# Optimization experiments

Measured on AMD Instinct MI355X. Metric: run time of the kernel, lower is better.

The kernel has to match this reference:

```python
import math
import jax, jax.numpy as jnp
import numpy as np

B, T, C, H = 2, 2048, 1024, 16  # batch, seq, embed, heads; head_dim = C//H = 64

def setup_inputs() -> dict:
    key = jax.random.key(0)
    k1, k2, k3 = jax.random.split(key, 3)
    x = jax.random.normal(k1, (B, T, C), dtype=jnp.float32)
    w_qkv = jax.random.normal(k2, (C, 3 * C), dtype=jnp.float32) * 0.02
    b_qkv = jnp.zeros((3 * C,), dtype=jnp.float32)
    w_proj = jax.random.normal(k3, (C, C), dtype=jnp.float32) * (0.02 / math.sqrt(2 * 24))
    b_proj = jnp.zeros((C,), dtype=jnp.float32)
    return {"x": x, "w_qkv": w_qkv, "b_qkv": b_qkv, "w_proj": w_proj, "b_proj": b_proj}

def reference(x, w_qkv, b_qkv, w_proj, b_proj):
    b, t, c = x.shape
    h = H
    qkv = x @ w_qkv + b_qkv  # [b, t, 3c]
    q, k, v = jnp.split(qkv, 3, axis=-1)
    # [b, t, c] -> [b, h, t, d]
    def heads(z):
        return z.reshape(b, t, h, c // h).transpose(0, 2, 1, 3)
    q, k, v = heads(q), heads(k), heads(v)
    # NOTE: source scales by sqrt(c) (full embed dim), not sqrt(head_dim)
    att = jnp.einsum("bhqd,bhkd->bhqk", q, k) / math.sqrt(c)
    # causal mask: -inf above diagonal
    mask = jnp.triu(jnp.full((t, t), -jnp.inf, dtype=att.dtype), k=1)
    att = att + mask
    att = jax.nn.softmax(att, axis=-1)
    out = jnp.einsum("bhqk,bhkd->bhqd", att, v)  # [b, h, t, d]
    out = out.transpose(0, 2, 1, 3).reshape(b, t, c)
    return out @ w_proj + b_proj
```

## Files before the change

kernel.cpp:

```cpp
#include <hip/hip_runtime.h>
#include <math.h>

#define BSZ 2
#define TSEQ 2048
#define CEMB 1024
#define NHEAD 16
#define HDIM 64

typedef float f32x4 __attribute__((ext_vector_type(4)));
typedef short bf16x8 __attribute__((ext_vector_type(8)));

typedef __attribute__((address_space(3))) char lds_char;
typedef __attribute__((address_space(1))) const char gbl_char;

__device__ __forceinline__ void g2l16(const void* g, void* l) {
    __builtin_amdgcn_global_load_lds((const gbl_char*)g, (lds_char*)l, 16, 0, 0);
}

__device__ __forceinline__ unsigned short f2bf(float x) {
    unsigned u = __float_as_uint(x);
    unsigned r = ((u >> 16) & 1u) + 0x7fffu;
    return (unsigned short)((u + r) >> 16);
}

__global__ __launch_bounds__(256) void conv_f32_bf16(
    const float* __restrict__ in, unsigned short* __restrict__ out)
{
    size_t i = ((size_t)blockIdx.x * 256 + threadIdx.x) * 8;
    float4 a = *(const float4*)(in + i);
    float4 b = *(const float4*)(in + i + 4);
    union { unsigned short u[8]; uint4 v; } pk;
    pk.u[0] = f2bf(a.x); pk.u[1] = f2bf(a.y); pk.u[2] = f2bf(a.z); pk.u[3] = f2bf(a.w);
    pk.u[4] = f2bf(b.x); pk.u[5] = f2bf(b.y); pk.u[6] = f2bf(b.z); pk.u[7] = f2bf(b.w);
    *(uint4*)(out + i) = pk.v;
}

__global__ __launch_bounds__(256) void conv_transpose_bf16(
    const float* __restrict__ w, unsigned short* __restrict__ wT, int K, int N)
{
    __shared__ float t[32][33];
    const int n0 = blockIdx.x * 32, k0 = blockIdx.y * 32;
    const int tx = threadIdx.x & 31, ty = threadIdx.x >> 5;
    #pragma unroll
    for (int i = 0; i < 4; ++i)
        t[ty + i * 8][tx] = w[(size_t)(k0 + ty + i * 8) * N + n0 + tx];
    __syncthreads();
    #pragma unroll
    for (int i = 0; i < 4; ++i) {
        int r = ty + i * 8;
        wT[(size_t)(n0 + r) * K + k0 + tx] = f2bf(t[tx][r]);
    }
}

template <int EPI>
__global__ __launch_bounds__(256) void gemm_mfma(
    const unsigned short* __restrict__ A, const unsigned short* __restrict__ BT,
    const float* __restrict__ bias,
    unsigned short* __restrict__ qo, unsigned short* __restrict__ ko,
    unsigned short* __restrict__ vo, float* __restrict__ fo,
    int M, int N, int K)
{
    __shared__ __align__(16) char sA[128 * 64 * 2];
    __shared__ __align__(16) char sB[128 * 64 * 2];

    const int tid = threadIdx.x;
    const int lane = tid & 63;
    const int wid = tid >> 6;
    const int wm = wid >> 1, wn = wid & 1;
    const int row0 = blockIdx.y * 128;
    const int col0 = blockIdx.x * 128;

    f32x4 acc[4][4] = {};

    for (int k0 = 0; k0 < K; k0 += 64) {
        __syncthreads();
        #pragma unroll
        for (int i = 0; i < 4; ++i) {
            int cid = i * 256 + tid;
            int row = cid >> 3, c2 = cid & 7;
            g2l16(&A[(size_t)(row0 + row) * K + k0 + ((c2 ^ (row & 7)) << 3)],
                  sA + ((i * 256 + (tid & 192)) << 4));
        }
        #pragma unroll
        for (int i = 0; i < 4; ++i) {
            int cid = i * 256 + tid;
            int row = cid >> 3, c2 = cid & 7;
            g2l16(&BT[(size_t)(col0 + row) * K + k0 + ((c2 ^ (row & 7)) << 3)],
                  sB + ((i * 256 + (tid & 192)) << 4));
        }
        __syncthreads();

        #pragma unroll
        for (int ks = 0; ks < 2; ++ks) {
            bf16x8 af[4], bf[4];
            #pragma unroll
            for (int mi = 0; mi < 4; ++mi) {
                int row = wm * 64 + mi * 16 + (lane & 15);
                int ch = ((lane >> 4) + 4 * ks) ^ (row & 7);
                af[mi] = *(const bf16x8*)(sA + row * 128 + (ch << 4));
            }
            #pragma unroll
            for (int ni = 0; ni < 4; ++ni) {
                int row = wn * 64 + ni * 16 + (lane & 15);
                int ch = ((lane >> 4) + 4 * ks) ^ (row & 7);
                bf[ni] = *(const bf16x8*)(sB + row * 128 + (ch << 4));
            }
            #pragma unroll
            for (int mi = 0; mi < 4; ++mi)
                #pragma unroll
                for (int ni = 0; ni < 4; ++ni)
                    acc[mi][ni] = __builtin_amdgcn_mfma_f32_16x16x32_bf16(
                        af[mi], bf[ni], acc[mi][ni], 0, 0, 0);
        }
    }

    #pragma unroll
    for (int mi = 0; mi < 4; ++mi) {
        const int rg = row0 + wm * 64 + mi * 16 + (lane >> 4) * 4;
        #pragma unroll
        for (int ni = 0; ni < 4; ++ni) {
            const int cg = col0 + wn * 64 + ni * 16 + (lane & 15);
            const float bv = bias[cg];
            if (EPI == 1) {
                #pragma unroll
                for (int r = 0; r < 4; ++r)
                    fo[(size_t)(rg + r) * N + cg] = acc[mi][ni][r] + bv;
            } else {
                const int region = col0 >> 10;
                if (region < 2) {
                    unsigned short* dst = region ? ko : qo;
                    const int nn = cg - (region << 10);
                    #pragma unroll
                    for (int r = 0; r < 4; ++r)
                        dst[(size_t)(rg + r) * CEMB + nn] = f2bf(acc[mi][ni][r] + bv);
                } else {
                    const int nloc = cg - 2048;
                    const int h = nloc >> 6, d = nloc & 63;
                    const int b = rg >> 11, t = rg & 2047;
                    ushort4 pk;
                    pk.x = f2bf(acc[mi][ni][0] + bv);
                    pk.y = f2bf(acc[mi][ni][1] + bv);
                    pk.z = f2bf(acc[mi][ni][2] + bv);
                    pk.w = f2bf(acc[mi][ni][3] + bv);
                    *(ushort4*)&vo[(((size_t)b * NHEAD + h) * HDIM + d) * TSEQ + t] = pk;
                }
            }
        }
    }
}

__global__ __launch_bounds__(256) void flash_mfma(
    const unsigned short* __restrict__ qb, const unsigned short* __restrict__ kb,
    const unsigned short* __restrict__ vt, unsigned short* __restrict__ ob)
{
    const int u = blockIdx.x >> 5;
    const int bh = blockIdx.x & 31;
    const int qt = (u & 1) ? (31 - (u >> 1)) : (u >> 1);
    const int b = bh >> 4, h = bh & 15;
    const int q0 = qt * 64;

    __shared__ __align__(16) char sQ[8192];
    __shared__ __align__(16) char sK[8192];
    __shared__ __align__(16) char sV[8192];
    __shared__ __align__(16) char sP[8192];

    const int tid = threadIdx.x;
    const int lane = tid & 63;
    const int wid = tid >> 6;
    const int g = lane >> 4;
    const int lr = lane & 15;
    const int q7 = lr & 7;

    #pragma unroll
    for (int i = 0; i < 2; ++i) {
        int cid = i * 256 + tid;
        int row = cid >> 3, c2 = cid & 7;
        g2l16(&qb[(size_t)(b * TSEQ + q0 + row) * CEMB + h * HDIM + ((c2 ^ (row & 7)) << 3)],
              sQ + ((i * 256 + (tid & 192)) << 4));
    }

    f32x4 o[4] = {};
    float mrow = -INFINITY, lrow = 0.f;
    const float c = 0.0450744431f;

    for (int kt = 0; kt <= qt; ++kt) {
        const int k0 = kt * 64;
        __syncthreads();
        #pragma unroll
        for (int i = 0; i < 2; ++i) {
            int cid = i * 256 + tid;
            int row = cid >> 3, c2 = cid & 7;
            g2l16(&kb[(size_t)(b * TSEQ + k0 + row) * CEMB + h * HDIM + ((c2 ^ (row & 7)) << 3)],
                  sK + ((i * 256 + (tid & 192)) << 4));
        }
        #pragma unroll
        for (int i = 0; i < 2; ++i) {
            int cid = i * 256 + tid;
            int row = cid >> 3, c2 = cid & 7;
            g2l16(&vt[(((size_t)b * NHEAD + h) * HDIM + row) * TSEQ + k0 + ((c2 ^ (row & 7)) << 3)],
                  sV + ((i * 256 + (tid & 192)) << 4));
        }
        __syncthreads();

        bf16x8 qf[2];
        #pragma unroll
        for (int ks = 0; ks < 2; ++ks) {
            int row = wid * 16 + lr;
            int ch = (g + 4 * ks) ^ q7;
            qf[ks] = *(const bf16x8*)(sQ + row * 128 + (ch << 4));
        }
        f32x4 s[4] = {};
        #pragma unroll
        for (int ni = 0; ni < 4; ++ni) {
            #pragma unroll
            for (int ks = 0; ks < 2; ++ks) {
                int row = ni * 16 + lr;
                int ch = (g + 4 * ks) ^ q7;
                bf16x8 kf = *(const bf16x8*)(sK + row * 128 + (ch << 4));
                s[ni] = __builtin_amdgcn_mfma_f32_16x16x32_bf16(kf, qf[ks], s[ni], 0, 0, 0);
            }
        }

        #pragma unroll
        for (int ni = 0; ni < 4; ++ni)
            #pragma unroll
            for (int r = 0; r < 4; ++r)
                s[ni][r] *= c;
        const int qrow_g = q0 + wid * 16 + lr;
        if (kt == qt) {
            #pragma unroll
            for (int ni = 0; ni < 4; ++ni)
                #pragma unroll
                for (int r = 0; r < 4; ++r)
                    if (k0 + ni * 16 + g * 4 + r > qrow_g) s[ni][r] = -INFINITY;
        }

        f32x4 m01, m23;
        #pragma unroll
        for (int r = 0; r < 4; ++r) {
            m01[r] = fmaxf(s[0][r], s[1][r]);
            m23[r] = fmaxf(s[2][r], s[3][r]);
        }
        float v = fmaxf(fmaxf(fmaxf(m01[0], m23[0]), fmaxf(m01[1], m23[1])),
                        fmaxf(fmaxf(m01[2], m23[2]), fmaxf(m01[3], m23[3])));
        v = fmaxf(v, __shfl_xor(v, 16));
        v = fmaxf(v, __shfl_xor(v, 32));

        if (!__all(v <= mrow + 8.f)) {
            const float mnew = fmaxf(mrow, v);
            const float sc = exp2f(mrow - mnew);
            lrow *= sc;
            #pragma unroll
            for (int ni = 0; ni < 4; ++ni)
                #pragma unroll
                for (int r = 0; r < 4; ++r)
                    o[ni][r] *= sc;
            mrow = mnew;
        }

        float ps = 0.f;
        #pragma unroll
        for (int ni = 0; ni < 4; ++ni) {
            ushort4 pk;
            #pragma unroll
            for (int r = 0; r < 4; ++r) {
                const float p = exp2f(s[ni][r] - mrow);
                ps += p;
                ((unsigned short*)&pk)[r] = f2bf(p);
            }
            const int ch = (2 * ni + (g >> 1)) ^ q7;
            *(uint2*)(sP + (wid * 16 + lr) * 128 + (ch << 4) + ((g & 1) << 3)) =
                *(const uint2*)&pk;
        }
        ps += __shfl_xor(ps, 16);
        ps += __shfl_xor(ps, 32);
        lrow += ps;

        asm volatile("s_waitcnt lgkmcnt(0)" ::: "memory");

        bf16x8 pf[2];
        #pragma unroll
        for (int ks = 0; ks < 2; ++ks) {
            int ch = (g + 4 * ks) ^ q7;
            pf[ks] = *(const bf16x8*)(sP + (wid * 16 + lr) * 128 + (ch << 4));
        }
        #pragma unroll
        for (int ni = 0; ni < 4; ++ni) {
            #pragma unroll
            for (int ks = 0; ks < 2; ++ks) {
                int row = ni * 16 + lr;
                int ch = (g + 4 * ks) ^ q7;
                bf16x8 vf = *(const bf16x8*)(sV + row * 128 + (ch << 4));
                o[ni] = __builtin_amdgcn_mfma_f32_16x16x32_bf16(vf, pf[ks], o[ni], 0, 0, 0);
            }
        }
    }

    const float linv = 1.f / lrow;
    __syncthreads();
    #pragma unroll
    for (int ni = 0; ni < 4; ++ni) {
        ushort4 pk;
        #pragma unroll
        for (int r = 0; r < 4; ++r)
            ((unsigned short*)&pk)[r] = f2bf(o[ni][r] * linv);
        const int ch = (2 * ni + (g >> 1)) ^ q7;
        *(uint2*)(sP + (wid * 16 + lr) * 128 + (ch << 4) + ((g & 1) << 3)) =
            *(const uint2*)&pk;
    }
    __syncthreads();
    #pragma unroll
    for (int i = 0; i < 2; ++i) {
        const int cid = i * 256 + tid;
        const int row = cid >> 3;
        const int ch = cid & 7;
        uint4 val = *(const uint4*)(sP + row * 128 + ((ch ^ (row & 7)) << 4));
        *(uint4*)&ob[(size_t)(b * TSEQ + q0 + row) * CEMB + h * HDIM + ch * 8] = val;
    }
}

extern "C" void kernel_launch(void* const* d_in, const int* in_sizes, int n_in,
                              void* d_out, int out_size, void* d_ws, size_t ws_size,
                              hipStream_t stream)
{
    (void)in_sizes; (void)n_in; (void)out_size; (void)ws_size;

    const float* x      = (const float*)d_in[0];
    const float* w_qkv  = (const float*)d_in[1];
    const float* b_qkv  = (const float*)d_in[2];
    const float* w_proj = (const float*)d_in[3];
    const float* b_proj = (const float*)d_in[4];
    float* out = (float*)d_out;

    const int M = BSZ * TSEQ;
    unsigned short* xb     = (unsigned short*)d_ws;
    unsigned short* wqkvT  = xb     + (size_t)M * CEMB;
    unsigned short* wprojT = wqkvT  + (size_t)3 * CEMB * CEMB;
    unsigned short* qbuf   = wprojT + (size_t)CEMB * CEMB;
    unsigned short* kbuf   = qbuf   + (size_t)M * CEMB;
    unsigned short* vbuf   = kbuf   + (size_t)M * CEMB;
    unsigned short* attb   = vbuf   + (size_t)M * CEMB;

    conv_f32_bf16<<<dim3((M * CEMB) / 2048), 256, 0, stream>>>(x, xb);
    conv_transpose_bf16<<<dim3(3 * CEMB / 32, CEMB / 32), 256, 0, stream>>>(
        w_qkv, wqkvT, CEMB, 3 * CEMB);
    conv_transpose_bf16<<<dim3(CEMB / 32, CEMB / 32), 256, 0, stream>>>(
        w_proj, wprojT, CEMB, CEMB);

    gemm_mfma<0><<<dim3(3 * CEMB / 128, M / 128), 256, 0, stream>>>(
        xb, wqkvT, b_qkv, qbuf, kbuf, vbuf, nullptr, M, 3 * CEMB, CEMB);

    flash_mfma<<<dim3(32 * 32), 256, 0, stream>>>(qbuf, kbuf, vbuf, attb);

    gemm_mfma<1><<<dim3(CEMB / 128, M / 128), 256, 0, stream>>>(
        attb, wprojT, b_proj, nullptr, nullptr, nullptr, out, M, CEMB, CEMB);
}
```

Measured before the change: 196.3 us.

## Double-buffer K/V tiles in flash attention and fold softmax scale into Q

The flash attention kernel now double-buffers the K and V tiles in LDS, prefetching the next tile while computing on the current one, with one barrier per iteration. Q fragments are loaded once into registers, reusing the sP buffer for staging. The softmax scale is folded into Q in the QKV GEMM epilogue, and the bf16 packing uses the hardware v_cvt_pk_bf16_f32 instruction. The block-index mapping is also reordered to change how causal query tiles spread across CUs. LDS use rises and the overlap depends on correct waits for the asynchronous global-to-LDS loads.

```diff
diff --git a/kernel.cpp b/kernel.cpp
--- a/kernel.cpp
+++ b/kernel.cpp
@@ -21,6 +21,12 @@
     unsigned u = __float_as_uint(x);
     unsigned r = ((u >> 16) & 1u) + 0x7fffu;
     return (unsigned short)((u + r) >> 16);
+}
+
+__device__ __forceinline__ unsigned pkbf(float lo, float hi) {
+    unsigned r;
+    asm("v_cvt_pk_bf16_f32 %0, %1, %2" : "=v"(r) : "v"(lo), "v"(hi));
+    return r;
 }
 
 __global__ __launch_bounds__(256) void conv_f32_bf16(
@@ -129,10 +135,11 @@
                 const int region = col0 >> 10;
                 if (region < 2) {
                     unsigned short* dst = region ? ko : qo;
+                    const float sc = region ? 1.f : 0.0450744431f;
                     const int nn = cg - (region << 10);
                     #pragma unroll
                     for (int r = 0; r < 4; ++r)
-                        dst[(size_t)(rg + r) * CEMB + nn] = f2bf(acc[mi][ni][r] + bv);
+                        dst[(size_t)(rg + r) * CEMB + nn] = f2bf((acc[mi][ni][r] + bv) * sc);
                 } else {
                     const int nloc = cg - 2048;
                     const int h = nloc >> 6, d = nloc & 63;
@@ -153,15 +160,18 @@
     const unsigned short* __restrict__ qb, const unsigned short* __restrict__ kb,
     const unsigned short* __restrict__ vt, unsigned short* __restrict__ ob)
 {
-    const int u = blockIdx.x >> 5;
-    const int bh = blockIdx.x & 31;
-    const int qt = (u & 1) ? (31 - (u >> 1)) : (u >> 1);
+    const int bid = blockIdx.x;
+    const int k4 = bid >> 8;
+    const int rem = bid & 255;
+    const int bh = rem >> 3;
+    const int bq = rem & 7;
+    const int qt = (k4 & 1) ? (31 - ((bq << 1) | (k4 >> 1)))
+                            : ((bq << 1) | (k4 >> 1));
     const int b = bh >> 4, h = bh & 15;
     const int q0 = qt * 64;
 
-    __shared__ __align__(16) char sQ[8192];
-    __shared__ __align__(16) char sK[8192];
-    __shared__ __align__(16) char sV[8192];
+    __shared__ __align__(16) char sK[2][8192];
+    __shared__ __align__(16) char sV[2][8192];
     __shared__ __align__(16) char sP[8192];
 
     const int tid = threadIdx.x;
@@ -176,39 +186,43 @@
         int cid = i * 256 + tid;
         int row = cid >> 3, c2 = cid & 7;
         g2l16(&qb[(size_t)(b * TSEQ + q0 + row) * CEMB + h * HDIM + ((c2 ^ (row & 7)) << 3)],
-              sQ + ((i * 256 + (tid & 192)) << 4));
-    }
+              sP + ((i * 256 + (tid & 192)) << 4));
+        g2l16(&kb[(size_t)(b * TSEQ + row) * CEMB + h * HDIM + ((c2 ^ (row & 7)) << 3)],
+              sK[0] + ((i * 256 + (tid & 192)) << 4));
+        g2l16(&vt[(((size_t)b * NHEAD + h) * HDIM + row) * TSEQ + ((c2 ^ (row & 7)) << 3)],
+              sV[0] + ((i * 256 + (tid & 192)) << 4));
+    }
+    __syncthreads();
+
+    bf16x8 qf[2];
+    #pragma unroll
+    for (int ks = 0; ks < 2; ++ks) {
+        int ch = (g + 4 * ks) ^ q7;
+        qf[ks] = *(const bf16x8*)(sP + (wid * 16 + lr) * 128 + (ch << 4));
+    }
+    __syncthreads();
 
     f32x4 o[4] = {};
     float mrow = -INFINITY, lrow = 0.f;
-    const float c = 0.0450744431f;
+    const int qrow_g = q0 + wid * 16 + lr;
 
     for (int kt = 0; kt <= qt; ++kt) {
-        const int k0 = kt * 64;
-        __syncthreads();
-        #pragma unroll
-        for (int i = 0; i < 2; ++i) {
-            int cid = i * 256 + tid;
-            int row = cid >> 3, c2 = cid & 7;
-            g2l16(&kb[(size_t)(b * TSEQ + k0 + row) * CEMB + h * HDIM + ((c2 ^ (row & 7)) << 3)],
-                  sK + ((i * 256 + (tid & 192)) << 4));
-        }
-        #pragma unroll
-        for (int i = 0; i < 2; ++i) {
-            int cid = i * 256 + tid;
-            int row = cid >> 3, c2 = cid & 7;
-            g2l16(&vt[(((size_t)b * NHEAD + h) * HDIM + row) * TSEQ + k0 + ((c2 ^ (row & 7)) << 3)],
-                  sV + ((i * 256 + (tid & 192)) << 4));
-        }
-        __syncthreads();
-
-        bf16x8 qf[2];
-        #pragma unroll
-        for (int ks = 0; ks < 2; ++ks) {
-            int row = wid * 16 + lr;
-            int ch = (g + 4 * ks) ^ q7;
-            qf[ks] = *(const bf16x8*)(sQ + row * 128 + (ch << 4));
-        }
+        const int cur = kt & 1;
+
+        if (kt < qt) {
+            const int k0n = (kt + 1) * 64;
+            const int nxt = cur ^ 1;
+            #pragma unroll
+            for (int i = 0; i < 2; ++i) {
+                int cid = i * 256 + tid;
+                int row = cid >> 3, c2 = cid & 7;
+                g2l16(&kb[(size_t)(b * TSEQ + k0n + row) * CEMB + h * HDIM + ((c2 ^ (row & 7)) << 3)],
+                      sK[nxt] + ((i * 256 + (tid & 192)) << 4));
+                g2l16(&vt[(((size_t)b * NHEAD + h) * HDIM + row) * TSEQ + k0n + ((c2 ^ (row & 7)) << 3)],
+                      sV[nxt] + ((i * 256 + (tid & 192)) << 4));
+            }
+        }
+
         f32x4 s[4] = {};
         #pragma unroll
         for (int ni = 0; ni < 4; ++ni) {
@@ -216,18 +230,13 @@
             for (int ks = 0; ks < 2; ++ks) {
                 int row = ni * 16 + lr;
                 int ch = (g + 4 * ks) ^ q7;
-                bf16x8 kf = *(const bf16x8*)(sK + row * 128 + (ch << 4));
+                bf16x8 kf = *(const bf16x8*)(sK[cur] + row * 128 + (ch << 4));
                 s[ni] = __builtin_amdgcn_mfma_f32_16x16x32_bf16(kf, qf[ks], s[ni], 0, 0, 0);
             }
         }
 
-        #pragma unroll
-        for (int ni = 0; ni < 4; ++ni)
-            #pragma unroll
-            for (int r = 0; r < 4; ++r)
-                s[ni][r] *= c;
-        const int qrow_g = q0 + wid * 16 + lr;
         if (kt == qt) {
+            const int k0 = kt * 64;
             #pragma unroll
             for (int ni = 0; ni < 4; ++ni)
                 #pragma unroll
@@ -235,14 +244,11 @@
                     if (k0 + ni * 16 + g * 4 + r > qrow_g) s[ni][r] = -INFINITY;
         }
 
-        f32x4 m01, m23;
-        #pragma unroll
-        for (int r = 0; r < 4; ++r) {
-            m01[r] = fmaxf(s[0][r], s[1][r]);
-            m23[r] = fmaxf(s[2][r], s[3][r]);
-        }
-        float v = fmaxf(fmaxf(fmaxf(m01[0], m23[0]), fmaxf(m01[1], m23[1])),
-                        fmaxf(fmaxf(m01[2], m23[2]), fmaxf(m01[3], m23[3])));
+        float v = s[0][0];
+        v = fmaxf(v, s[0][1]); v = fmaxf(v, s[0][2]); v = fmaxf(v, s[0][3]);
+        v = fmaxf(v, s[1][0]); v = fmaxf(v, s[1][1]); v = fmaxf(v, s[1][2]); v = fmaxf(v, s[1][3]);
+        v = fmaxf(v, s[2][0]); v = fmaxf(v, s[2][1]); v = fmaxf(v, s[2][2]); v = fmaxf(v, s[2][3]);
+        v = fmaxf(v, s[3][0]); v = fmaxf(v, s[3][1]); v = fmaxf(v, s[3][2]); v = fmaxf(v, s[3][3]);
         v = fmaxf(v, __shfl_xor(v, 16));
         v = fmaxf(v, __shfl_xor(v, 32));
 
@@ -261,16 +267,16 @@
         float ps = 0.f;
         #pragma unroll
         for (int ni = 0; ni < 4; ++ni) {
-            ushort4 pk;
-            #pragma unroll
-            for (int r = 0; r < 4; ++r) {
-                const float p = exp2f(s[ni][r] - mrow);
-                ps += p;
-                ((unsigned short*)&pk)[r] = f2bf(p);
-            }
+            const float p0 = exp2f(s[ni][0] - mrow);
+            const float p1 = exp2f(s[ni][1] - mrow);
+            const float p2 = exp2f(s[ni][2] - mrow);
+            const float p3 = exp2f(s[ni][3] - mrow);
+            ps += (p0 + p1) + (p2 + p3);
+            uint2 w;
+            w.x = pkbf(p0, p1);
+            w.y = pkbf(p2, p3);
             const int ch = (2 * ni + (g >> 1)) ^ q7;
-            *(uint2*)(sP + (wid * 16 + lr) * 128 + (ch << 4) + ((g & 1) << 3)) =
-                *(const uint2*)&pk;
+            *(uint2*)(sP + (wid * 16 + lr) * 128 + (ch << 4) + ((g & 1) << 3)) = w;
         }
         ps += __shfl_xor(ps, 16);
         ps += __shfl_xor(ps, 32);
@@ -290,23 +296,22 @@
             for (int ks = 0; ks < 2; ++ks) {
                 int row = ni * 16 + lr;
                 int ch = (g + 4 * ks) ^ q7;
-                bf16x8 vf = *(const bf16x8*)(sV + row * 128 + (ch << 4));
+                bf16x8 vf = *(const bf16x8*)(sV[cur] + row * 128 + (ch << 4));
                 o[ni] = __builtin_amdgcn_mfma_f32_16x16x32_bf16(vf, pf[ks], o[ni], 0, 0, 0);
             }
         }
+
+        __syncthreads();
     }
 
     const float linv = 1.f / lrow;
-    __syncthreads();
     #pragma unroll
     for (int ni = 0; ni < 4; ++ni) {
-        ushort4 pk;
-        #pragma unroll
-        for (int r = 0; r < 4; ++r)
-            ((unsigned short*)&pk)[r] = f2bf(o[ni][r] * linv);
+        uint2 w;
+        w.x = pkbf(o[ni][0] * linv, o[ni][1] * linv);
+        w.y = pkbf(o[ni][2] * linv, o[ni][3] * linv);
         const int ch = (2 * ni + (g >> 1)) ^ q7;
-        *(uint2*)(sP + (wid * 16 + lr) * 128 + (ch << 4) + ((g & 1) << 3)) =
-            *(const uint2*)&pk;
+        *(uint2*)(sP + (wid * 16 + lr) * 128 + (ch << 4) + ((g & 1) << 3)) = w;
     }
     __syncthreads();
     #pragma unroll
```

Result: faster. 188.0 us (-4.2%).
